# Optimization experiments

Hardware: AMD Instinct MI355X
Metric: run time of the kernel (lower is better)

The kernel has to match this reference:

```python
import jax, jax.numpy as jnp
import numpy as np

N_NODES = 100000
N_EDGES = 1600000
NODE_DIM = 32
EDGE_DIM = 16
OUT_DIM = 32


def setup_inputs() -> dict:
    key = jax.random.key(0)
    ks = jax.random.split(key, 8)
    D = NODE_DIM + EDGE_DIM  # 48
    return {
        "y": jax.random.normal(ks[0], (N_NODES, NODE_DIM), dtype=jnp.float32),
        "ex": jax.random.normal(ks[1], (N_EDGES, EDGE_DIM), dtype=jnp.float32),
        "W1": jax.random.normal(ks[2], (D, D), dtype=jnp.float32) / np.sqrt(D),
        "b1": jax.random.normal(ks[3], (D,), dtype=jnp.float32) * 0.01,
        "W2": jax.random.normal(ks[4], (OUT_DIM, D), dtype=jnp.float32) / np.sqrt(D),
        "b2": jax.random.normal(ks[5], (OUT_DIM,), dtype=jnp.float32) * 0.01,
        "src": jax.random.randint(ks[6], (N_EDGES,), 0, N_NODES, dtype=jnp.int32),
        "dst": jax.random.randint(ks[7], (N_EDGES,), 0, N_NODES, dtype=jnp.int32),
    }


def reference(y, ex, W1, b1, W2, b2, src, dst):
    n_nodes = y.shape[0]
    # per-edge message: ReLU(Linear(concat(y[src], e_x)))  -> [E, node_dim+edge_dim]
    feat = jnp.concatenate([y[src], ex], axis=1)
    m = jax.nn.relu(feat @ W1.T + b1)
    # mean scatter-reduce onto destination nodes (0 for isolated nodes, DGL semantics)
    s = jax.ops.segment_sum(m, dst, num_segments=n_nodes)
    cnt = jax.ops.segment_sum(jnp.ones((m.shape[0],), m.dtype), dst, num_segments=n_nodes)
    z = jnp.where(cnt[:, None] > 0, s / jnp.maximum(cnt, 1.0)[:, None], 0.0)
    # node update: ReLU(Linear(z)) -> [N, out_dim]
    h = jax.nn.relu(z @ W2.T + b2)
    return h
```

## Files before the change

### kernel.cpp

```cpp
#include <hip/hip_runtime.h>

#define NODE_DIM 32
#define EDGE_DIM 16
#define DD 48
#define OUT_DIM 32
#define MAXDEG 64
#define STAGED 32
#define NXCD 8
#define NPW 8

typedef _Float16 f16x8 __attribute__((ext_vector_type(8)));
typedef float f32x4 __attribute__((ext_vector_type(4)));

__global__ __launch_bounds__(256)
void prep_scatter_kernel(const int* __restrict__ dst, const int* __restrict__ src,
                         int* __restrict__ cursor, int2* __restrict__ meta,
                         int E, int NP, int K, int G,
                         const float* __restrict__ y, _Float16* __restrict__ yh,
                         int CBy, const float* __restrict__ ex,
                         _Float16* __restrict__ exh, int N) {
    const int b  = blockIdx.x;
    const int g  = b >> 3;
    const int r8 = b & 7;
    const long long gk = (long long)g * K;
    const int s0 = (int)(gk / G);
    const int s1 = (int)((gk + K) / G);

    if (s1 > s0) {
        const int base = s0 * 2048 + threadIdx.x * 8;
        if (base >= E) return;
        int dv[8], sv[8];
        if (base + 8 <= E) {
            *reinterpret_cast<int4*>(dv)     = *reinterpret_cast<const int4*>(dst + base);
            *reinterpret_cast<int4*>(dv + 4) = *reinterpret_cast<const int4*>(dst + base + 4);
            *reinterpret_cast<int4*>(sv)     = *reinterpret_cast<const int4*>(src + base);
            *reinterpret_cast<int4*>(sv + 4) = *reinterpret_cast<const int4*>(src + base + 4);
        } else {
#pragma unroll
            for (int i = 0; i < 8; ++i) {
                dv[i] = (base + i < E) ? dst[base + i] : -1;
                sv[i] = (base + i < E) ? src[base + i] : 0;
            }
        }
#pragma unroll
        for (int i = 0; i < 8; ++i) {
            const int d = dv[i];
            if (d >= 0 && (d & (NXCD - 1)) == r8 && base + i < E) {
                int pos = atomicAdd(&cursor[r8 * NP + (d >> 3)], 1);
                if (pos < MAXDEG)
                    meta[(size_t)d * MAXDEG + pos] = make_int2(base + i, sv[i]);
            }
        }
        return;
    }

    int cb = (g - s0) * 8 + r8;
    if (cb < CBy) {
        size_t i = ((size_t)cb * 256 + threadIdx.x) * 8;
        if (i < (size_t)N * NODE_DIM) {
            const float4* p = reinterpret_cast<const float4*>(y + i);
            const float4 a = p[0], c = p[1];
            f16x8 h = {(_Float16)a.x, (_Float16)a.y, (_Float16)a.z, (_Float16)a.w,
                       (_Float16)c.x, (_Float16)c.y, (_Float16)c.z, (_Float16)c.w};
            *reinterpret_cast<f16x8*>(yh + i) = h;
        }
        return;
    }
    cb -= CBy;
    size_t i = ((size_t)cb * 256 + threadIdx.x) * 8;
    if (i < (size_t)E * EDGE_DIM) {
        const float4* p = reinterpret_cast<const float4*>(ex + i);
        const float4 a = p[0], c = p[1];
        f16x8 h = {(_Float16)a.x, (_Float16)a.y, (_Float16)a.z, (_Float16)a.w,
                   (_Float16)c.x, (_Float16)c.y, (_Float16)c.z, (_Float16)c.w};
        *reinterpret_cast<f16x8*>(exh + i) = h;
    }
}

__global__ __launch_bounds__(256)
void fused_kernel(const _Float16* __restrict__ yh, const _Float16* __restrict__ exh,
                  const float* __restrict__ W1, const float* __restrict__ b1,
                  const float* __restrict__ W2, const float* __restrict__ b2,
                  const int* __restrict__ cursor, const int2* __restrict__ meta,
                  float* __restrict__ out, int N, int NP) {
    __shared__ int2 mlds[4][NPW][STAGED];
    __shared__ _Float16 zl[4][NPW][64];

    const int wave = threadIdx.x >> 6;
    const int lane = threadIdx.x & 63;
    const int col = lane & 15;
    const int kg  = lane >> 4;

    f16x8 Blo[3], Bhi[3];
#pragma unroll
    for (int t = 0; t < 3; ++t) {
        const float* wr = W1 + (size_t)(t * 16 + col) * DD;
#pragma unroll
        for (int j = 0; j < 8; ++j) {
            Blo[t][j] = (_Float16)wr[kg * 8 + j];
            Bhi[t][j] = (_Float16)0.f;
        }
        if (kg < 2) {
#pragma unroll
            for (int j = 0; j < 8; ++j)
                Bhi[t][j] = (_Float16)wr[NODE_DIM + kg * 8 + j];
        }
        if (kg == 3) Bhi[t][7] = (_Float16)b1[t * 16 + col];
    }

    const int nb0 = (blockIdx.x * 4 + wave) * NPW;

    int dgv = 0;
    if (lane < NPW) {
        const int n = nb0 + lane;
        if (n < N) dgv = cursor[(n & (NXCD - 1)) * NP + (n >> 3)];
    }

#pragma unroll
    for (int ni = 0; ni < NPW; ++ni) {
        const int cnt_i = min(__shfl(dgv, ni), STAGED);
        const int n = nb0 + ni;
        if (lane < STAGED)
            mlds[wave][ni][lane] = (lane < cnt_i && n < N)
                                       ? meta[(size_t)n * MAXDEG + lane]
                                       : make_int2(0, 0);
    }
    __builtin_amdgcn_wave_barrier();

    f16x8 ahiC;
#pragma unroll
    for (int j = 0; j < 8; ++j) ahiC[j] = (_Float16)0.f;
    if (kg == 3) ahiC[7] = (_Float16)1.f;

#pragma unroll 2
    for (int ni = 0; ni < NPW; ++ni) {
        const int n = nb0 + ni;
        const int dg = __shfl(dgv, ni);
        const int cnt = min(dg, MAXDEG);

        float pacc0 = 0.f, pacc1 = 0.f, pacc2 = 0.f;

        {
            const bool v0 = col < cnt;
            const int2 md0 = mlds[wave][ni][col];
            f16x8 alo0 = *reinterpret_cast<const f16x8*>(
                yh + (size_t)md0.y * NODE_DIM + kg * 8);
            f16x8 ahi0 = ahiC;
            if (kg < 2)
                ahi0 = *reinterpret_cast<const f16x8*>(
                    exh + (size_t)md0.x * EDGE_DIM + kg * 8);

            f16x8 alo1, ahi1;
            const bool haveG1 = cnt > 16;
            if (haveG1) {
                const int2 md1 = mlds[wave][ni][16 + col];
                alo1 = *reinterpret_cast<const f16x8*>(
                    yh + (size_t)md1.y * NODE_DIM + kg * 8);
                ahi1 = ahiC;
                if (kg < 2)
                    ahi1 = *reinterpret_cast<const f16x8*>(
                        exh + (size_t)md1.x * EDGE_DIM + kg * 8);
            }

            if (!v0) {
#pragma unroll
                for (int j = 0; j < 8; ++j) { alo0[j] = (_Float16)0.f; ahi0[j] = (_Float16)0.f; }
            }
#pragma unroll
            for (int t = 0; t < 3; ++t) {
                f32x4 c = {0.f, 0.f, 0.f, 0.f};
                c = __builtin_amdgcn_mfma_f32_16x16x32_f16(alo0, Blo[t], c, 0, 0, 0);
                c = __builtin_amdgcn_mfma_f32_16x16x32_f16(ahi0, Bhi[t], c, 0, 0, 0);
#pragma unroll
                for (int r = 0; r < 4; ++r) {
                    const float v = fmaxf(c[r], 0.f);
                    if (t == 0) pacc0 += v;
                    else if (t == 1) pacc1 += v;
                    else pacc2 += v;
                }
            }

            if (haveG1) {
                const bool v1 = (16 + col) < cnt;
                if (!v1) {
#pragma unroll
                    for (int j = 0; j < 8; ++j) { alo1[j] = (_Float16)0.f; ahi1[j] = (_Float16)0.f; }
                }
#pragma unroll
                for (int t = 0; t < 3; ++t) {
                    f32x4 c = {0.f, 0.f, 0.f, 0.f};
                    c = __builtin_amdgcn_mfma_f32_16x16x32_f16(alo1, Blo[t], c, 0, 0, 0);
                    c = __builtin_amdgcn_mfma_f32_16x16x32_f16(ahi1, Bhi[t], c, 0, 0, 0);
#pragma unroll
                    for (int r = 0; r < 4; ++r) {
                        const float v = fmaxf(c[r], 0.f);
                        if (t == 0) pacc0 += v;
                        else if (t == 1) pacc1 += v;
                        else pacc2 += v;
                    }
                }
            }
        }

        if (cnt > STAGED) {
            const int ngroups = (cnt + 15) >> 4;
            for (int g = 2; g < ngroups; ++g) {
                const int row = g * 16 + col;
                const bool valid = row < cnt;
                const int2 md = valid ? meta[(size_t)n * MAXDEG + row]
                                      : make_int2(0, 0);
                f16x8 alo = *reinterpret_cast<const f16x8*>(
                    yh + (size_t)md.y * NODE_DIM + kg * 8);
                f16x8 ahi = ahiC;
                if (kg < 2)
                    ahi = *reinterpret_cast<const f16x8*>(
                        exh + (size_t)md.x * EDGE_DIM + kg * 8);
                if (!valid) {
#pragma unroll
                    for (int j = 0; j < 8; ++j) { alo[j] = (_Float16)0.f; ahi[j] = (_Float16)0.f; }
                }
#pragma unroll
                for (int t = 0; t < 3; ++t) {
                    f32x4 c = {0.f, 0.f, 0.f, 0.f};
                    c = __builtin_amdgcn_mfma_f32_16x16x32_f16(alo, Blo[t], c, 0, 0, 0);
                    c = __builtin_amdgcn_mfma_f32_16x16x32_f16(ahi, Bhi[t], c, 0, 0, 0);
#pragma unroll
                    for (int r = 0; r < 4; ++r) {
                        const float v = fmaxf(c[r], 0.f);
                        if (t == 0) pacc0 += v;
                        else if (t == 1) pacc1 += v;
                        else pacc2 += v;
                    }
                }
            }
        }

        pacc0 += __shfl_xor(pacc0, 16); pacc0 += __shfl_xor(pacc0, 32);
        pacc1 += __shfl_xor(pacc1, 16); pacc1 += __shfl_xor(pacc1, 32);
        pacc2 += __shfl_xor(pacc2, 16); pacc2 += __shfl_xor(pacc2, 32);

        if (n < N) {
            const float inv = (dg > 0) ? 1.f / (float)dg : 0.f;
            if (lane < 16) {
                zl[wave][ni][lane]      = (_Float16)(pacc0 * inv);
                zl[wave][ni][lane + 16] = (_Float16)(pacc1 * inv);
                zl[wave][ni][lane + 32] = (_Float16)(pacc2 * inv);
            }
            if (lane < 8) {
                const unsigned int v = (lane == 0) ? 0x00003C00u : 0u;
                *reinterpret_cast<unsigned int*>(&zl[wave][ni][48 + lane * 2]) = v;
            }
        } else if (lane < 32) {
            *reinterpret_cast<unsigned int*>(&zl[wave][ni][lane * 2]) = 0u;
        }
    }

    f16x8 Wf[2][2];
#pragma unroll
    for (int t = 0; t < 2; ++t) {
#pragma unroll
        for (int c = 0; c < 2; ++c) {
            f16x8 v;
#pragma unroll
            for (int j = 0; j < 8; ++j) {
                const int k = c * 32 + kg * 8 + j;
                float w = 0.f;
                if (k < DD)       w = W2[(size_t)(t * 16 + col) * DD + k];
                else if (k == DD) w = b2[t * 16 + col];
                v[j] = (_Float16)w;
            }
            Wf[t][c] = v;
        }
    }

    __builtin_amdgcn_wave_barrier();
    const _Float16* zr = &zl[wave][col & (NPW - 1)][0];
    const f16x8 A0 = *reinterpret_cast<const f16x8*>(zr + kg * 8);
    const f16x8 A1 = *reinterpret_cast<const f16x8*>(zr + 32 + kg * 8);

#pragma unroll
    for (int t = 0; t < 2; ++t) {
        f32x4 h = {0.f, 0.f, 0.f, 0.f};
        h = __builtin_amdgcn_mfma_f32_16x16x32_f16(A0, Wf[t][0], h, 0, 0, 0);
        h = __builtin_amdgcn_mfma_f32_16x16x32_f16(A1, Wf[t][1], h, 0, 0, 0);
#pragma unroll
        for (int r = 0; r < 4; ++r) {
            const int mrow = kg * 4 + r;
            const int node = nb0 + mrow;
            if (mrow < NPW && node < N)
                out[(size_t)node * OUT_DIM + t * 16 + col] = fmaxf(h[r], 0.f);
        }
    }
}

extern "C" void kernel_launch(void* const* d_in, const int* in_sizes, int n_in,
                              void* d_out, int out_size, void* d_ws, size_t ws_size,
                              hipStream_t stream) {
    const float* y  = (const float*)d_in[0];
    const float* ex = (const float*)d_in[1];
    const float* W1 = (const float*)d_in[2];
    const float* b1 = (const float*)d_in[3];
    const float* W2 = (const float*)d_in[4];
    const float* b2 = (const float*)d_in[5];
    const int* src  = (const int*)d_in[6];
    const int* dst  = (const int*)d_in[7];

    const int N = in_sizes[0] / NODE_DIM;
    const int E = in_sizes[6];
    const int NP = (N + NXCD - 1) / NXCD;
    const int NC = ((NXCD * NP + 3) / 4) * 4;

    int* cursor = (int*)d_ws;
    size_t off  = ((size_t)NC * sizeof(int) + 255) & ~(size_t)255;
    int2* meta  = (int2*)((char*)d_ws + off);
    _Float16* yh = (_Float16*)((char*)meta + (size_t)N * MAXDEG * sizeof(int2));
    _Float16* exh = (_Float16*)((char*)yh + (size_t)N * NODE_DIM * sizeof(_Float16));

    const int CBy = (N * NODE_DIM / 8 + 255) / 256;
    const int CBe = (E * EDGE_DIM / 8 + 255) / 256;
    const int K   = (E + 2047) / 2048;
    const int CG  = (CBy + CBe + 7) / 8;
    const int G   = K + CG;

    hipMemsetAsync(cursor, 0, (size_t)NC * sizeof(int), stream);

    prep_scatter_kernel<<<G * 8, 256, 0, stream>>>(dst, src, cursor, meta,
                                                   E, NP, K, G,
                                                   y, yh, CBy, ex, exh, N);

    const int NB = (N + NPW * 4 - 1) / (NPW * 4);
    fused_kernel<<<NB, 256, 0, stream>>>(yh, exh, W1, b1, W2, b2,
                                         cursor, meta, (float*)d_out, N, NP);
}
```

Before: 169.3 us.

## Reorder edge features into destination-bucketed fp16 layout via separate kernel

Removes the fp32-to-fp16 conversion of edge features from the prep kernel. A new reorder kernel gathers each edge's features by the bucketed edge id, converts them to fp16, and writes them contiguously per destination slot. The fused kernel then reads edge features with coalesced, slot-indexed loads instead of random gathers through meta. The cost is an extra kernel launch and an extra padded buffer of N*64*16 halfs that is written and then read back, including slots that stay empty.

After: 202.1 us. 19.4% more time.

```diff
diff --git a/kernel.cpp b/kernel.cpp
--- a/kernel.cpp
+++ b/kernel.cpp
@@ -17,8 +17,7 @@
                          int* __restrict__ cursor, int2* __restrict__ meta,
                          int E, int NP, int K, int G,
                          const float* __restrict__ y, _Float16* __restrict__ yh,
-                         int CBy, const float* __restrict__ ex,
-                         _Float16* __restrict__ exh, int N) {
+                         int CBy, int N) {
     const int b  = blockIdx.x;
     const int g  = b >> 3;
     const int r8 = b & 7;
@@ -64,21 +63,34 @@
                        (_Float16)c.x, (_Float16)c.y, (_Float16)c.z, (_Float16)c.w};
             *reinterpret_cast<f16x8*>(yh + i) = h;
         }
-        return;
-    }
-    cb -= CBy;
-    size_t i = ((size_t)cb * 256 + threadIdx.x) * 8;
-    if (i < (size_t)E * EDGE_DIM) {
-        const float4* p = reinterpret_cast<const float4*>(ex + i);
-        const float4 a = p[0], c = p[1];
-        f16x8 h = {(_Float16)a.x, (_Float16)a.y, (_Float16)a.z, (_Float16)a.w,
-                   (_Float16)c.x, (_Float16)c.y, (_Float16)c.z, (_Float16)c.w};
-        *reinterpret_cast<f16x8*>(exh + i) = h;
     }
 }
 
 __global__ __launch_bounds__(256)
-void fused_kernel(const _Float16* __restrict__ yh, const _Float16* __restrict__ exh,
+void reorder_kernel(const float* __restrict__ ex, const int* __restrict__ cursor,
+                    const int2* __restrict__ meta, _Float16* __restrict__ exb,
+                    int N, int NP) {
+    const int gid = blockIdx.x * 256 + threadIdx.x;
+    const int n = gid >> 6;
+    const int slot = gid & 63;
+    if (n >= N) return;
+    const int dg = cursor[(n & (NXCD - 1)) * NP + (n >> 3)];
+    if (slot < min(dg, MAXDEG)) {
+        const int eid = meta[(size_t)n * MAXDEG + slot].x;
+        const float4* ep = reinterpret_cast<const float4*>(ex + (size_t)eid * EDGE_DIM);
+        const float4 a = ep[0], b = ep[1], c = ep[2], d = ep[3];
+        f16x8 h0 = {(_Float16)a.x, (_Float16)a.y, (_Float16)a.z, (_Float16)a.w,
+                    (_Float16)b.x, (_Float16)b.y, (_Float16)b.z, (_Float16)b.w};
+        f16x8 h1 = {(_Float16)c.x, (_Float16)c.y, (_Float16)c.z, (_Float16)c.w,
+                    (_Float16)d.x, (_Float16)d.y, (_Float16)d.z, (_Float16)d.w};
+        f16x8* o = reinterpret_cast<f16x8*>(exb + ((size_t)n * MAXDEG + slot) * EDGE_DIM);
+        o[0] = h0;
+        o[1] = h1;
+    }
+}
+
+__global__ __launch_bounds__(256)
+void fused_kernel(const _Float16* __restrict__ yh, const _Float16* __restrict__ exb,
                   const float* __restrict__ W1, const float* __restrict__ b1,
                   const float* __restrict__ W2, const float* __restrict__ b2,
                   const int* __restrict__ cursor, const int2* __restrict__ meta,
@@ -135,6 +147,7 @@
 #pragma unroll 2
     for (int ni = 0; ni < NPW; ++ni) {
         const int n = nb0 + ni;
+        const size_t ebase = (size_t)min(n, N - 1) * MAXDEG;
         const int dg = __shfl(dgv, ni);
         const int cnt = min(dg, MAXDEG);
 
@@ -142,24 +155,24 @@
 
         {
             const bool v0 = col < cnt;
+            f16x8 ahi0 = ahiC;
+            if (kg < 2)
+                ahi0 = *reinterpret_cast<const f16x8*>(
+                    exb + (ebase + col) * EDGE_DIM + kg * 8);
             const int2 md0 = mlds[wave][ni][col];
             f16x8 alo0 = *reinterpret_cast<const f16x8*>(
                 yh + (size_t)md0.y * NODE_DIM + kg * 8);
-            f16x8 ahi0 = ahiC;
-            if (kg < 2)
-                ahi0 = *reinterpret_cast<const f16x8*>(
-                    exh + (size_t)md0.x * EDGE_DIM + kg * 8);
 
             f16x8 alo1, ahi1;
             const bool haveG1 = cnt > 16;
             if (haveG1) {
+                ahi1 = ahiC;
+                if (kg < 2)
+                    ahi1 = *reinterpret_cast<const f16x8*>(
+                        exb + (ebase + 16 + col) * EDGE_DIM + kg * 8);
                 const int2 md1 = mlds[wave][ni][16 + col];
                 alo1 = *reinterpret_cast<const f16x8*>(
                     yh + (size_t)md1.y * NODE_DIM + kg * 8);
-                ahi1 = ahiC;
-                if (kg < 2)
-                    ahi1 = *reinterpret_cast<const f16x8*>(
-                        exh + (size_t)md1.x * EDGE_DIM + kg * 8);
             }
 
             if (!v0) {
@@ -214,7 +227,7 @@
                 f16x8 ahi = ahiC;
                 if (kg < 2)
                     ahi = *reinterpret_cast<const f16x8*>(
-                        exh + (size_t)md.x * EDGE_DIM + kg * 8);
+                        exb + (ebase + min(row, MAXDEG - 1)) * EDGE_DIM + kg * 8);
                 if (!valid) {
 #pragma unroll
                     for (int j = 0; j < 8; ++j) { alo[j] = (_Float16)0.f; ahi[j] = (_Float16)0.f; }
@@ -313,22 +326,23 @@
     int* cursor = (int*)d_ws;
     size_t off  = ((size_t)NC * sizeof(int) + 255) & ~(size_t)255;
     int2* meta  = (int2*)((char*)d_ws + off);
-    _Float16* yh = (_Float16*)((char*)meta + (size_t)N * MAXDEG * sizeof(int2));
-    _Float16* exh = (_Float16*)((char*)yh + (size_t)N * NODE_DIM * sizeof(_Float16));
+    _Float16* yh  = (_Float16*)((char*)meta + (size_t)N * MAXDEG * sizeof(int2));
+    _Float16* exb = (_Float16*)((char*)yh + (size_t)N * NODE_DIM * sizeof(_Float16));
 
     const int CBy = (N * NODE_DIM / 8 + 255) / 256;
-    const int CBe = (E * EDGE_DIM / 8 + 255) / 256;
     const int K   = (E + 2047) / 2048;
-    const int CG  = (CBy + CBe + 7) / 8;
+    const int CG  = (CBy + 7) / 8;
     const int G   = K + CG;
 
     hipMemsetAsync(cursor, 0, (size_t)NC * sizeof(int), stream);
 
     prep_scatter_kernel<<<G * 8, 256, 0, stream>>>(dst, src, cursor, meta,
-                                                   E, NP, K, G,
-                                                   y, yh, CBy, ex, exh, N);
+                                                   E, NP, K, G, y, yh, CBy, N);
+
+    const int RB = (N * 64 + 255) / 256;
+    reorder_kernel<<<RB, 256, 0, stream>>>(ex, cursor, meta, exb, N, NP);
 
     const int NB = (N + NPW * 4 - 1) / (NPW * 4);
-    fused_kernel<<<NB, 256, 0, stream>>>(yh, exh, W1, b1, W2, b2,
+    fused_kernel<<<NB, 256, 0, stream>>>(yh, exb, W1, b1, W2, b2,
                                          cursor, meta, (float*)d_out, N, NP);
 }
```
